# Kernel optimization log

Hardware: AMD Instinct MI355X
Metric: run time of the kernel (lower is better)

## Reference

```python
import jax, jax.numpy as jnp
import numpy as np

EPS = 1e-3  # keras BatchNormalization default epsilon


def _ngf(atoms, bonds, edges, W, b):
    """NeuralGraphHidden: neighbor gather + per-degree dense.
    atoms [B,N,Fa], bonds [B,N,D,Fb], edges [B,N,D] (-1 padded),
    W [D+1, Fa+Fb, width], b [D+1, width] -> [B,N,width]."""
    B, N, Fa = atoms.shape
    D = edges.shape[-1]
    deg = jnp.sum(edges != -1, axis=-1)  # [B,N] atom degrees
    # zero-row padded lookup table so edge index -1 gathers zeros
    apad = jnp.concatenate([jnp.zeros((B, 1, Fa), atoms.dtype), atoms], axis=1)
    neigh = jax.vmap(lambda a, e: a[e])(apad, edges + 1)  # [B,N,D,Fa]
    summed_atom = atoms + neigh.sum(axis=2)  # include_self=True
    summed_bond = bonds.sum(axis=2)
    feats = jnp.concatenate([summed_atom, summed_bond], axis=-1)  # [B,N,Fa+Fb]
    # dense transform for every degree, then select by actual degree
    all_out = jnp.einsum('bnf,dfw->bdnw', feats, W) + b[None, :, None, :]
    mask = (deg[:, None, :] == jnp.arange(D + 1)[None, :, None]).astype(atoms.dtype)
    return jnp.einsum('bdnw,bdn->bnw', all_out, mask)


def _bn(x, g, beta, m, v):
    return g * (x - m) * jax.lax.rsqrt(v + EPS) + beta


def setup_inputs() -> dict:
    key = jax.random.key(0)
    ks = jax.random.split(key, 32)
    B, N, D, Fa, Fb = 1024, 60, 5, 62, 6
    widths = [128, 128, 128]
    KSZ, FILT = 16, 128

    atoms = jax.random.normal(ks[0], (B, N, Fa), jnp.float32)
    bonds = jax.random.uniform(ks[1], (B, N, D, Fb), dtype=jnp.float32)
    edges = jax.random.randint(ks[2], (B, N, D), -1, N).astype(jnp.int32)

    def glorot(k, shape):
        s = jnp.sqrt(2.0 / (shape[-2] + shape[-1])).astype(jnp.float32)
        return jax.random.normal(k, shape, jnp.float32) * s

    inp = dict(atoms=atoms, bonds=bonds, edges=edges)
    fins = [Fa + Fb, widths[0] + Fb, widths[1] + Fb]
    for i in range(3):
        inp['W%d' % (i + 1)] = glorot(ks[3 + i], (D + 1, fins[i], widths[i]))
        inp['b%d' % (i + 1)] = 0.01 * jax.random.normal(ks[6 + i], (D + 1, widths[i]), jnp.float32)
    inp['Wc'] = glorot(ks[9], (KSZ, widths[2], FILT))
    for i, c in enumerate([widths[0], widths[1], widths[2], FILT]):
        inp['bn%d_g' % (i + 1)] = 1.0 + 0.1 * jax.random.normal(ks[10 + i], (c,), jnp.float32)
        inp['bn%d_b' % (i + 1)] = 0.1 * jax.random.normal(ks[14 + i], (c,), jnp.float32)
        inp['bn%d_m' % (i + 1)] = 0.1 * jax.random.normal(ks[18 + i], (c,), jnp.float32)
        inp['bn%d_v' % (i + 1)] = jax.random.uniform(ks[22 + i], (c,), jnp.float32, 0.5, 1.5)
    return inp


def reference(atoms, bonds, edges, W1, b1, W2, b2, W3, b3, Wc,
              bn1_g, bn1_b, bn1_m, bn1_v, bn2_g, bn2_b, bn2_m, bn2_v,
              bn3_g, bn3_b, bn3_m, bn3_v, bn4_g, bn4_b, bn4_m, bn4_v):
    x = jax.nn.relu(_bn(_ngf(atoms, bonds, edges, W1, b1), bn1_g, bn1_b, bn1_m, bn1_v))
    x = jax.nn.relu(_bn(_ngf(x, bonds, edges, W2, b2), bn2_g, bn2_b, bn2_m, bn2_v))
    x = jax.nn.relu(_bn(_ngf(x, bonds, edges, W3, b3), bn3_g, bn3_b, bn3_m, bn3_v))
    # Conv1D over the atom axis, VALID padding, no bias
    x = jax.lax.conv_general_dilated(x, Wc, window_strides=(1,), padding='VALID',
                                     dimension_numbers=('NWC', 'WIO', 'NWC'))
    x = jax.nn.relu(_bn(x, bn4_g, bn4_b, bn4_m, bn4_v))
    # dropout is identity at inference
    return x
```

## Files before the change

kernel.cpp:

```cpp
#include <hip/hip_runtime.h>
#include <hip/hip_bf16.h>

typedef __attribute__((ext_vector_type(8))) short bf16x8;
typedef __attribute__((ext_vector_type(4))) short short4v;
typedef __attribute__((ext_vector_type(4))) float f32x4;
typedef unsigned short u16;

static constexpr size_t OFF_BN   = 0;
static constexpr size_t OFF_SH2  = 4096;
static constexpr size_t OFF_BSUM = 13312;
static constexpr size_t OFF_WT1  = 750592;
static constexpr size_t OFF_WT2  = 898048;
static constexpr size_t OFF_WT3  = 1143808;
static constexpr size_t OFF_WCF  = 1389568;

__device__ __forceinline__ float bf2f(u16 r) {
  union { unsigned u; float f; } cv; cv.u = ((unsigned)r) << 16; return cv.f;
}
__device__ __forceinline__ u16 f2bf(float x) {
  __hip_bfloat16 h = __float2bfloat16(x); return *(u16*)&h;
}
__device__ __forceinline__ int xswz(int n, int c) {
  return n * 128 + ((((c >> 3) ^ (n & 7)) << 3) | (c & 7));
}
__device__ __forceinline__ int fswz(int n, int c) {
  return n * 160 + ((((c >> 3) ^ ((n >> 1) & 3)) << 3) | (c & 7));
}

__global__ __launch_bounds__(512) void bn_prep(
    const float* g1, const float* be1, const float* m1, const float* v1,
    const float* g2, const float* be2, const float* m2, const float* v2,
    const float* g3, const float* be3, const float* m3, const float* v3,
    const float* g4, const float* be4, const float* m4, const float* v4,
    const float* bb1, const float* bb2, const float* bb3,
    float* __restrict__ scale, float* __restrict__ shift,
    float* __restrict__ shift2) {
  int bid = blockIdx.x, t = threadIdx.x;
  if (bid == 0) {
    const float* gs[4] = {g1, g2, g3, g4};
    const float* bs[4] = {be1, be2, be3, be4};
    const float* ms[4] = {m1, m2, m3, m4};
    const float* vs[4] = {v1, v2, v3, v4};
    int l = t >> 7, ch = t & 127;
    float g = gs[l][ch], be = bs[l][ch], m = ms[l][ch], v = vs[l][ch];
    float sc = g / sqrtf(v + 1e-3f);
    scale[t] = sc;
    shift[t] = be - m * sc;
  } else if (t < 384) {
    int d = bid - 1;
    const float* gs[3] = {g1, g2, g3};
    const float* bs[3] = {be1, be2, be3};
    const float* ms[3] = {m1, m2, m3};
    const float* vs[3] = {v1, v2, v3};
    const float* bl[3] = {bb1, bb2, bb3};
    int ll = t >> 7, f = t & 127;
    float g = gs[ll][f], be = bs[ll][f], m = ms[ll][f], v = vs[ll][f];
    float sc = g / sqrtf(v + 1e-3f);
    float sh = be - m * sc;
    shift2[ll * 768 + d * 128 + f] = bl[ll][d * 128 + f] * sc + sh;
  }
}

__global__ __launch_bounds__(256) void bsum_prep(const float* __restrict__ bonds,
                                                 u16* __restrict__ bsum) {
  int a = blockIdx.x * 256 + threadIdx.x;
  const float* p = bonds + (size_t)a * 30;
  float s[6] = {0.f, 0.f, 0.f, 0.f, 0.f, 0.f};
  #pragma unroll
  for (int d = 0; d < 5; ++d)
    #pragma unroll
    for (int j = 0; j < 6; ++j) s[j] += p[d * 6 + j];
  #pragma unroll
  for (int j = 0; j < 6; ++j) bsum[(size_t)a * 6 + j] = f2bf(s[j]);
}

template <int FIN, int KSTEPS>
__global__ __launch_bounds__(256) void wtf_prep(const float* __restrict__ W,
                                                u16* __restrict__ wtf) {
  int v = blockIdx.x * 256 + threadIdx.x;
  if (v >= 6 * KSTEPS * 8 * 64) return;
  int lane = v & 63;
  int ftile = (v >> 6) & 7;
  int ks = (v >> 9) % KSTEPS;
  int d = (v >> 9) / KSTEPS;
  int f = ftile * 16 + (lane & 15);
  int k0 = ks * 32 + (lane >> 4) * 8;
  bf16x8 o;
  #pragma unroll
  for (int i = 0; i < 8; ++i) {
    int k = k0 + i;
    float x = (k < FIN) ? W[((size_t)d * FIN + k) * 128 + f] : 0.f;
    o[i] = (short)f2bf(x);
  }
  *reinterpret_cast<bf16x8*>(&wtf[(size_t)v * 8]) = o;
}

__global__ __launch_bounds__(512) void wcf_prep(const float* __restrict__ Wc,
                                                u16* __restrict__ wcf) {
  int v = blockIdx.x * 512 + threadIdx.x;
  int lane = v & 63;
  int ftile = (v >> 6) & 7;
  int ks = v >> 9;
  int f = ftile * 16 + (lane & 15);
  int k0 = ks * 32 + (lane >> 4) * 8;
  int tap = k0 >> 7, ch0 = k0 & 127;
  bf16x8 o;
  #pragma unroll
  for (int i = 0; i < 8; ++i)
    o[i] = (short)f2bf(Wc[((size_t)tap * 128 + ch0 + i) * 128 + f]);
  *reinterpret_cast<bf16x8*>(&wcf[(size_t)v * 8]) = o;
}

template <int CIN, int KSTEPS>
__device__ __forceinline__ void ngf_layer_dev(
    u16* __restrict__ xb, u16* __restrict__ feats,
    const int* __restrict__ eds, const int* __restrict__ degs,
    const int* __restrict__ presentS,
    const u16* __restrict__ bsum_b,
    const u16* __restrict__ wtf,
    const float* __restrict__ sc_l, const float* __restrict__ sh2_l,
    int tid, int lane, int wid) {
  constexpr int CW = (CIN <= 64) ? 64 : 128;
  for (int i = tid; i < 60 * CW; i += 256) {
    int n = i / CW, c = i % CW;
    if (c < CIN) {
      float v = bf2f(xb[xswz(n, c)]);
      #pragma unroll
      for (int d = 0; d < 5; ++d) {
        int e = eds[n * 5 + d];
        if (e >= 0) v += bf2f(xb[xswz(e, c)]);
      }
      feats[fswz(n, c)] = f2bf(v);
    }
  }
  for (int i = tid; i < 360; i += 256) {
    int n = i / 6, c = CIN + (i % 6);
    feats[fswz(n, c)] = bsum_b[i];
  }
  __syncthreads();

  const int pres = *presentS;
  const int rgrp = lane >> 4;
  const int fr = lane & 15;
  const int f0 = wid * 32;

  for (int d = 0; d < 6; ++d) {
    if (!(pres & (1 << d))) continue;
    f32x4 acc[4][2];
    #pragma unroll
    for (int mt = 0; mt < 4; ++mt)
      #pragma unroll
      for (int nt = 0; nt < 2; ++nt) acc[mt][nt] = (f32x4){0.f, 0.f, 0.f, 0.f};
    const u16* __restrict__ wd = wtf + (size_t)d * KSTEPS * 4096;
    bf16x8 bcur[2], bnxt[2];
    #pragma unroll
    for (int nt = 0; nt < 2; ++nt)
      bcur[nt] = *reinterpret_cast<const bf16x8*>(
          &wd[(((size_t)0 * 8 + wid * 2 + nt) * 64 + lane) * 8]);
    #pragma unroll
    for (int ks = 0; ks < KSTEPS; ++ks) {
      if (ks + 1 < KSTEPS) {
        #pragma unroll
        for (int nt = 0; nt < 2; ++nt)
          bnxt[nt] = *reinterpret_cast<const bf16x8*>(
              &wd[((((size_t)ks + 1) * 8 + wid * 2 + nt) * 64 + lane) * 8]);
      }
      bf16x8 a[4];
      #pragma unroll
      for (int mt = 0; mt < 4; ++mt) {
        int r = mt * 16 + fr;
        int u = (ks * 4 + rgrp) ^ ((fr >> 1) & 3);
        a[mt] = *reinterpret_cast<const bf16x8*>(&feats[r * 160 + u * 8]);
      }
      #pragma unroll
      for (int mt = 0; mt < 4; ++mt)
        #pragma unroll
        for (int nt = 0; nt < 2; ++nt)
          acc[mt][nt] = __builtin_amdgcn_mfma_f32_16x16x32_bf16(a[mt], bcur[nt],
                                                                acc[mt][nt], 0, 0, 0);
      #pragma unroll
      for (int nt = 0; nt < 2; ++nt) bcur[nt] = bnxt[nt];
    }
    float s0 = sc_l[f0 + fr],      h0 = sh2_l[d * 128 + f0 + fr];
    float s1 = sc_l[f0 + 16 + fr], h1 = sh2_l[d * 128 + f0 + 16 + fr];
    #pragma unroll
    for (int mt = 0; mt < 4; ++mt) {
      #pragma unroll
      for (int j = 0; j < 4; ++j) {
        int n = mt * 16 + rgrp * 4 + j;
        if (n < 60 && degs[n] == d) {
          xb[xswz(n, f0 + fr)]      = f2bf(fmaxf(acc[mt][0][j] * s0 + h0, 0.f));
          xb[xswz(n, f0 + 16 + fr)] = f2bf(fmaxf(acc[mt][1][j] * s1 + h1, 0.f));
        }
      }
    }
  }
  __syncthreads();
}

__global__ __launch_bounds__(256, 4) void mega(
    const float* __restrict__ atoms, const int* __restrict__ edges_g,
    const u16* __restrict__ bsum, const u16* __restrict__ wt1,
    const u16* __restrict__ wt2, const u16* __restrict__ wt3,
    const u16* __restrict__ wcf, const float* __restrict__ scale,
    const float* __restrict__ shift, const float* __restrict__ shift2,
    float* __restrict__ out) {
  __shared__ u16 xb[64 * 128];
  __shared__ u16 feats[64 * 160];
  __shared__ int eds[300];
  __shared__ int degs[64];
  __shared__ int presentS;
  const int b = blockIdx.x, tid = threadIdx.x;
  const int lane = tid & 63;
  const int wid = __builtin_amdgcn_readfirstlane(tid >> 6);

  if (tid == 0) presentS = 0;
  for (int i = tid; i < 300; i += 256) eds[i] = edges_g[b * 300 + i];
  {
    short4v* fz = (short4v*)feats;
    for (int i = tid; i < 64 * 160 / 4; i += 256) fz[i] = (short4v){0, 0, 0, 0};
  }
  for (int i = tid; i < 60 * 64; i += 256) {
    int n = i >> 6, c = i & 63;
    if (c < 62) xb[xswz(n, c)] = f2bf(atoms[(size_t)b * 3720 + n * 62 + c]);
  }
  __syncthreads();

  if (tid < 64) {
    int dg = 7;
    if (tid < 60) {
      dg = 0;
      #pragma unroll
      for (int d = 0; d < 5; ++d) dg += (eds[tid * 5 + d] >= 0);
      atomicOr(&presentS, 1 << dg);
    }
    degs[tid] = dg;
  }

  const u16* bsum_b = bsum + (size_t)b * 360;
  ngf_layer_dev<62, 3>(xb, feats, eds, degs, &presentS, bsum_b, wt1,
                       scale + 0, shift2 + 0, tid, lane, wid);
  ngf_layer_dev<128, 5>(xb, feats, eds, degs, &presentS, bsum_b, wt2,
                        scale + 128, shift2 + 768, tid, lane, wid);
  ngf_layer_dev<128, 5>(xb, feats, eds, degs, &presentS, bsum_b, wt3,
                        scale + 256, shift2 + 1536, tid, lane, wid);

  {
    const int fr = lane & 15;
    const int rgrp = lane >> 4;
    const int f0 = wid * 32;
    f32x4 cacc[3][2];
    #pragma unroll
    for (int rt = 0; rt < 3; ++rt)
      #pragma unroll
      for (int ct = 0; ct < 2; ++ct) cacc[rt][ct] = (f32x4){0.f, 0.f, 0.f, 0.f};

    bf16x8 br[2][2], ar[2][3];
    auto loadB = [&](int ks, int slot) {
      #pragma unroll
      for (int nt = 0; nt < 2; ++nt)
        br[slot][nt] = *reinterpret_cast<const bf16x8*>(
            &wcf[(((size_t)ks * 8 + wid * 2 + nt) * 64 + lane) * 8]);
    };
    auto loadA = [&](int ks, int slot) {
      int rowadd = ks >> 2;
      int unit = ((ks & 3) << 2) + rgrp;
      #pragma unroll
      for (int rt = 0; rt < 3; ++rt) {
        int arow = rt * 16 + fr + rowadd;
        int uo = unit ^ (arow & 7);
        ar[slot][rt] = *reinterpret_cast<const bf16x8*>(&xb[arow * 128 + uo * 8]);
      }
    };
    loadB(0, 0); loadB(1, 1); loadA(0, 0);
    #pragma unroll 2
    for (int ks = 0; ks < 64; ++ks) {
      if (ks < 63) loadA(ks + 1, (ks + 1) & 1);
      #pragma unroll
      for (int rt = 0; rt < 3; ++rt)
        #pragma unroll
        for (int ct = 0; ct < 2; ++ct)
          cacc[rt][ct] = __builtin_amdgcn_mfma_f32_16x16x32_bf16(
              ar[ks & 1][rt], br[ks & 1][ct], cacc[rt][ct], 0, 0, 0);
      if (ks < 62) loadB(ks + 2, ks & 1);
    }

    #pragma unroll
    for (int ct = 0; ct < 2; ++ct) {
      int f = f0 + ct * 16 + fr;
      float sc = scale[384 + f], sh = shift[384 + f];
      #pragma unroll
      for (int rt = 0; rt < 3; ++rt) {
        #pragma unroll
        for (int j = 0; j < 4; ++j) {
          int t = rt * 16 + rgrp * 4 + j;
          if (t < 45) {
            float y = fmaxf(cacc[rt][ct][j] * sc + sh, 0.f);
            out[((size_t)b * 45 + t) * 128 + f] = y;
          }
        }
      }
    }
  }
}

extern "C" void kernel_launch(void* const* d_in, const int* in_sizes, int n_in,
                              void* d_out, int out_size, void* d_ws, size_t ws_size,
                              hipStream_t stream) {
  const float* atoms = (const float*)d_in[0];
  const float* bonds = (const float*)d_in[1];
  const int*   edges = (const int*)d_in[2];
  const float* W1 = (const float*)d_in[3]; const float* b1 = (const float*)d_in[4];
  const float* W2 = (const float*)d_in[5]; const float* b2 = (const float*)d_in[6];
  const float* W3 = (const float*)d_in[7]; const float* b3 = (const float*)d_in[8];
  const float* Wc = (const float*)d_in[9];

  char* ws = (char*)d_ws;
  float* scale  = (float*)(ws + OFF_BN);
  float* shift  = scale + 512;
  float* shift2 = (float*)(ws + OFF_SH2);
  u16*   bsum   = (u16*)(ws + OFF_BSUM);
  u16*   wt1    = (u16*)(ws + OFF_WT1);
  u16*   wt2    = (u16*)(ws + OFF_WT2);
  u16*   wt3    = (u16*)(ws + OFF_WT3);
  u16*   wcf    = (u16*)(ws + OFF_WCF);

  bn_prep<<<7, 512, 0, stream>>>(
      (const float*)d_in[10], (const float*)d_in[11], (const float*)d_in[12], (const float*)d_in[13],
      (const float*)d_in[14], (const float*)d_in[15], (const float*)d_in[16], (const float*)d_in[17],
      (const float*)d_in[18], (const float*)d_in[19], (const float*)d_in[20], (const float*)d_in[21],
      (const float*)d_in[22], (const float*)d_in[23], (const float*)d_in[24], (const float*)d_in[25],
      b1, b2, b3, scale, shift, shift2);
  bsum_prep<<<240, 256, 0, stream>>>(bonds, bsum);
  wcf_prep<<<64, 512, 0, stream>>>(Wc, wcf);
  wtf_prep<68, 3><<<36, 256, 0, stream>>>(W1, wt1);
  wtf_prep<134, 5><<<60, 256, 0, stream>>>(W2, wt2);
  wtf_prep<134, 5><<<60, 256, 0, stream>>>(W3, wt3);

  mega<<<1024, 256, 0, stream>>>(atoms, edges, bsum, wt1, wt2, wt3, wcf,
                                 scale, shift, shift2, (float*)d_out);
}
```

Measured before the change: 218.6 us.

## Replace scalar neighbor gather with adjacency-matrix MFMA and fuse prep kernels

The per-element neighbor gather-sum is replaced by building a per-molecule 60x60 adjacency count matrix (self plus edges) in shared memory and computing the aggregation as a bf16 MFMA matmul against a transposed activation buffer. The per-degree dense stage is transposed (weights as the A operand, features as B), the layer-3 output is written in the row layout the conv expects, and edges and degrees are stored as bytes to shrink shared memory. The six preprocessing launches are merged into one kernel, and the bond sums are staged through shared memory. Rounding the aggregated sums to bf16 before the dense stage slightly changes numerics.

```diff
diff --git a/kernel.cpp b/kernel.cpp
--- a/kernel.cpp
+++ b/kernel.cpp
@@ -5,6 +5,7 @@
 typedef __attribute__((ext_vector_type(4))) short short4v;
 typedef __attribute__((ext_vector_type(4))) float f32x4;
 typedef unsigned short u16;
+typedef unsigned char u8;
 
 static constexpr size_t OFF_BN   = 0;
 static constexpr size_t OFF_SH2  = 4096;
@@ -20,65 +21,12 @@
 __device__ __forceinline__ u16 f2bf(float x) {
   __hip_bfloat16 h = __float2bfloat16(x); return *(u16*)&h;
 }
-__device__ __forceinline__ int xswz(int n, int c) {
-  return n * 128 + ((((c >> 3) ^ (n & 7)) << 3) | (c & 7));
-}
-__device__ __forceinline__ int fswz(int n, int c) {
-  return n * 160 + ((((c >> 3) ^ ((n >> 1) & 3)) << 3) | (c & 7));
-}
-
-__global__ __launch_bounds__(512) void bn_prep(
-    const float* g1, const float* be1, const float* m1, const float* v1,
-    const float* g2, const float* be2, const float* m2, const float* v2,
-    const float* g3, const float* be3, const float* m3, const float* v3,
-    const float* g4, const float* be4, const float* m4, const float* v4,
-    const float* bb1, const float* bb2, const float* bb3,
-    float* __restrict__ scale, float* __restrict__ shift,
-    float* __restrict__ shift2) {
-  int bid = blockIdx.x, t = threadIdx.x;
-  if (bid == 0) {
-    const float* gs[4] = {g1, g2, g3, g4};
-    const float* bs[4] = {be1, be2, be3, be4};
-    const float* ms[4] = {m1, m2, m3, m4};
-    const float* vs[4] = {v1, v2, v3, v4};
-    int l = t >> 7, ch = t & 127;
-    float g = gs[l][ch], be = bs[l][ch], m = ms[l][ch], v = vs[l][ch];
-    float sc = g / sqrtf(v + 1e-3f);
-    scale[t] = sc;
-    shift[t] = be - m * sc;
-  } else if (t < 384) {
-    int d = bid - 1;
-    const float* gs[3] = {g1, g2, g3};
-    const float* bs[3] = {be1, be2, be3};
-    const float* ms[3] = {m1, m2, m3};
-    const float* vs[3] = {v1, v2, v3};
-    const float* bl[3] = {bb1, bb2, bb3};
-    int ll = t >> 7, f = t & 127;
-    float g = gs[ll][f], be = bs[ll][f], m = ms[ll][f], v = vs[ll][f];
-    float sc = g / sqrtf(v + 1e-3f);
-    float sh = be - m * sc;
-    shift2[ll * 768 + d * 128 + f] = bl[ll][d * 128 + f] * sc + sh;
-  }
-}
-
-__global__ __launch_bounds__(256) void bsum_prep(const float* __restrict__ bonds,
-                                                 u16* __restrict__ bsum) {
-  int a = blockIdx.x * 256 + threadIdx.x;
-  const float* p = bonds + (size_t)a * 30;
-  float s[6] = {0.f, 0.f, 0.f, 0.f, 0.f, 0.f};
-  #pragma unroll
-  for (int d = 0; d < 5; ++d)
-    #pragma unroll
-    for (int j = 0; j < 6; ++j) s[j] += p[d * 6 + j];
-  #pragma unroll
-  for (int j = 0; j < 6; ++j) bsum[(size_t)a * 6 + j] = f2bf(s[j]);
-}
-
-template <int FIN, int KSTEPS>
-__global__ __launch_bounds__(256) void wtf_prep(const float* __restrict__ W,
-                                                u16* __restrict__ wtf) {
-  int v = blockIdx.x * 256 + threadIdx.x;
-  if (v >= 6 * KSTEPS * 8 * 64) return;
+__device__ __forceinline__ int xts(int c, int n) {
+  return c * 64 + (((n >> 3) ^ (c & 7)) << 3) + (n & 7);
+}
+
+__device__ __forceinline__ void emit_wt(u16* dst, const float* W, int FIN, int FIN_A,
+                                        int CB, int KSTEPS, int v) {
   int lane = v & 63;
   int ftile = (v >> 6) & 7;
   int ks = (v >> 9) % KSTEPS;
@@ -89,108 +37,222 @@
   #pragma unroll
   for (int i = 0; i < 8; ++i) {
     int k = k0 + i;
-    float x = (k < FIN) ? W[((size_t)d * FIN + k) * 128 + f] : 0.f;
+    int src = (k < FIN_A) ? k : (k >= CB && k < CB + 6) ? (FIN_A + k - CB) : -1;
+    float x = (src >= 0) ? W[((size_t)d * FIN + src) * 128 + f] : 0.f;
     o[i] = (short)f2bf(x);
   }
-  *reinterpret_cast<bf16x8*>(&wtf[(size_t)v * 8]) = o;
-}
-
-__global__ __launch_bounds__(512) void wcf_prep(const float* __restrict__ Wc,
-                                                u16* __restrict__ wcf) {
-  int v = blockIdx.x * 512 + threadIdx.x;
-  int lane = v & 63;
-  int ftile = (v >> 6) & 7;
-  int ks = v >> 9;
-  int f = ftile * 16 + (lane & 15);
-  int k0 = ks * 32 + (lane >> 4) * 8;
-  int tap = k0 >> 7, ch0 = k0 & 127;
-  bf16x8 o;
-  #pragma unroll
-  for (int i = 0; i < 8; ++i)
-    o[i] = (short)f2bf(Wc[((size_t)tap * 128 + ch0 + i) * 128 + f]);
-  *reinterpret_cast<bf16x8*>(&wcf[(size_t)v * 8]) = o;
-}
-
-template <int CIN, int KSTEPS>
-__device__ __forceinline__ void ngf_layer_dev(
-    u16* __restrict__ xb, u16* __restrict__ feats,
-    const int* __restrict__ eds, const int* __restrict__ degs,
-    const int* __restrict__ presentS,
-    const u16* __restrict__ bsum_b,
-    const u16* __restrict__ wtf,
-    const float* __restrict__ sc_l, const float* __restrict__ sh2_l,
-    int tid, int lane, int wid) {
-  constexpr int CW = (CIN <= 64) ? 64 : 128;
-  for (int i = tid; i < 60 * CW; i += 256) {
-    int n = i / CW, c = i % CW;
-    if (c < CIN) {
-      float v = bf2f(xb[xswz(n, c)]);
-      #pragma unroll
-      for (int d = 0; d < 5; ++d) {
-        int e = eds[n * 5 + d];
-        if (e >= 0) v += bf2f(xb[xswz(e, c)]);
-      }
-      feats[fswz(n, c)] = f2bf(v);
+  *reinterpret_cast<bf16x8*>(&dst[(size_t)v * 8]) = o;
+}
+
+__global__ __launch_bounds__(256) void prep(
+    const float* __restrict__ bonds, const float* __restrict__ Wc,
+    const float* __restrict__ W1, const float* __restrict__ W2, const float* __restrict__ W3,
+    const float* g1, const float* be1, const float* m1, const float* v1,
+    const float* g2, const float* be2, const float* m2, const float* v2,
+    const float* g3, const float* be3, const float* m3, const float* v3,
+    const float* g4, const float* be4, const float* m4, const float* v4,
+    const float* bb1, const float* bb2, const float* bb3,
+    float* __restrict__ scale, float* __restrict__ shift, float* __restrict__ shift2,
+    u16* __restrict__ bsum, u16* __restrict__ wt1, u16* __restrict__ wt2,
+    u16* __restrict__ wt3, u16* __restrict__ wcf) {
+  __shared__ float sb[3840];
+  const int b = blockIdx.x, tid = threadIdx.x;
+  if (b < 480) {
+    const int base = b * 128;
+    const float4* src = (const float4*)(bonds + (size_t)base * 30);
+    for (int i = tid; i < 960; i += 256) ((float4*)sb)[i] = src[i];
+    __syncthreads();
+    if (tid < 128) {
+      float s[6] = {0.f, 0.f, 0.f, 0.f, 0.f, 0.f};
+      #pragma unroll
+      for (int d = 0; d < 5; ++d)
+        #pragma unroll
+        for (int j = 0; j < 6; ++j) s[j] += sb[tid * 30 + d * 6 + j];
+      #pragma unroll
+      for (int j = 0; j < 6; ++j) bsum[(size_t)(base + tid) * 6 + j] = f2bf(s[j]);
+    }
+  } else if (b < 608) {
+    int v = (b - 480) * 256 + tid;
+    int lane = v & 63, ftile = (v >> 6) & 7, ks = v >> 9;
+    int f = ftile * 16 + (lane & 15);
+    int k0 = ks * 32 + (lane >> 4) * 8;
+    int tap = k0 >> 7, ch0 = k0 & 127;
+    bf16x8 o;
+    #pragma unroll
+    for (int i = 0; i < 8; ++i)
+      o[i] = (short)f2bf(Wc[((size_t)tap * 128 + ch0 + i) * 128 + f]);
+    *reinterpret_cast<bf16x8*>(&wcf[(size_t)v * 8]) = o;
+  } else if (b < 644) {
+    emit_wt(wt1, W1, 68, 62, 64, 3, (b - 608) * 256 + tid);
+  } else if (b < 704) {
+    emit_wt(wt2, W2, 134, 128, 128, 5, (b - 644) * 256 + tid);
+  } else if (b < 764) {
+    emit_wt(wt3, W3, 134, 128, 128, 5, (b - 704) * 256 + tid);
+  } else if (b < 766) {
+    int idx = (b - 764) * 256 + tid;
+    const float* gs[4] = {g1, g2, g3, g4};
+    const float* bs[4] = {be1, be2, be3, be4};
+    const float* ms[4] = {m1, m2, m3, m4};
+    const float* vs[4] = {v1, v2, v3, v4};
+    int l = idx >> 7, ch = idx & 127;
+    float sc = gs[l][ch] / sqrtf(vs[l][ch] + 1e-3f);
+    scale[idx] = sc;
+    shift[idx] = bs[l][ch] - ms[l][ch] * sc;
+  } else {
+    int i = (b - 766) * 256 + tid;
+    if (i < 2304) {
+      const float* G[3] = {g1, g2, g3};
+      const float* Be[3] = {be1, be2, be3};
+      const float* M[3] = {m1, m2, m3};
+      const float* V[3] = {v1, v2, v3};
+      const float* Bl[3] = {bb1, bb2, bb3};
+      int ll = i / 768, r = i % 768, f = r & 127;
+      float sc = G[ll][f] / sqrtf(V[ll][f] + 1e-3f);
+      float sh = Be[ll][f] - M[ll][f] * sc;
+      shift2[i] = Bl[ll][r] * sc + sh;
+    }
+  }
+}
+
+template <int MPW, int CB, int KSTEPS, bool TOCONV>
+__device__ __forceinline__ void layer(
+    u16* __restrict__ feats, u16* __restrict__ xbt,
+    const u8* __restrict__ S8, const u8* __restrict__ degs8,
+    const int* __restrict__ presentS, const u16* __restrict__ bsum_b,
+    const u16* __restrict__ wtf, const float* __restrict__ sc_l,
+    const float* __restrict__ sh2_l, int tid, int lane, int wid) {
+  const int fr = lane & 15, rg = lane >> 4;
+
+  bf16x8 sf[4][2];
+  #pragma unroll
+  for (int nt = 0; nt < 4; ++nt) {
+    #pragma unroll
+    for (int ks = 0; ks < 2; ++ks) {
+      int n = nt * 16 + fr, m0 = ks * 32 + rg * 8;
+      const unsigned* wp = (const unsigned*)(S8 + n * 64 + m0);
+      unsigned lo = wp[0], hi = wp[1];
+      bf16x8 v;
+      #pragma unroll
+      for (int i = 0; i < 4; ++i) v[i] = (short)f2bf((float)((lo >> (i * 8)) & 255u));
+      #pragma unroll
+      for (int i = 0; i < 4; ++i) v[4 + i] = (short)f2bf((float)((hi >> (i * 8)) & 255u));
+      sf[nt][ks] = v;
+    }
+  }
+
+  f32x4 gacc[MPW][4];
+  #pragma unroll
+  for (int mt = 0; mt < MPW; ++mt)
+    #pragma unroll
+    for (int nt = 0; nt < 4; ++nt) gacc[mt][nt] = (f32x4){0.f, 0.f, 0.f, 0.f};
+  #pragma unroll
+  for (int mt = 0; mt < MPW; ++mt) {
+    const int c = (wid * MPW + mt) * 16 + fr;
+    #pragma unroll
+    for (int ks = 0; ks < 2; ++ks) {
+      const int m0 = ks * 32 + rg * 8;
+      bf16x8 a = *reinterpret_cast<const bf16x8*>(
+          &xbt[c * 64 + (((m0 >> 3) ^ (c & 7)) << 3)]);
+      #pragma unroll
+      for (int nt = 0; nt < 4; ++nt)
+        gacc[mt][nt] = __builtin_amdgcn_mfma_f32_16x16x32_bf16(a, sf[nt][ks],
+                                                               gacc[mt][nt], 0, 0, 0);
+    }
+  }
+  #pragma unroll
+  for (int mt = 0; mt < MPW; ++mt) {
+    const int c0 = (wid * MPW + mt) * 16 + rg * 4;
+    const int uu = c0 >> 3;
+    #pragma unroll
+    for (int nt = 0; nt < 4; ++nt) {
+      const int n = nt * 16 + fr;
+      if (n < 60) {
+        short4v p;
+        #pragma unroll
+        for (int j = 0; j < 4; ++j) p[j] = (short)f2bf(gacc[mt][nt][j]);
+        *reinterpret_cast<short4v*>(
+            &feats[n * 160 + ((uu ^ (n & 7)) << 3) + (c0 & 7)]) = p;
+      }
     }
   }
   for (int i = tid; i < 360; i += 256) {
-    int n = i / 6, c = CIN + (i % 6);
-    feats[fswz(n, c)] = bsum_b[i];
+    int n = i / 6, c = CB + (i % 6);
+    int u = c >> 3;
+    int uu2 = (u < 16) ? (u ^ (n & 7)) : u;
+    feats[n * 160 + (uu2 << 3) + (c & 7)] = bsum_b[i];
   }
   __syncthreads();
 
   const int pres = *presentS;
-  const int rgrp = lane >> 4;
-  const int fr = lane & 15;
-  const int f0 = wid * 32;
+  int dg[4];
+  #pragma unroll
+  for (int nt = 0; nt < 4; ++nt) dg[nt] = degs8[nt * 16 + fr];
+  float4 scv[2];
+  #pragma unroll
+  for (int mt = 0; mt < 2; ++mt)
+    scv[mt] = *reinterpret_cast<const float4*>(&sc_l[(wid * 2 + mt) * 16 + rg * 4]);
 
   for (int d = 0; d < 6; ++d) {
     if (!(pres & (1 << d))) continue;
-    f32x4 acc[4][2];
-    #pragma unroll
-    for (int mt = 0; mt < 4; ++mt)
-      #pragma unroll
-      for (int nt = 0; nt < 2; ++nt) acc[mt][nt] = (f32x4){0.f, 0.f, 0.f, 0.f};
+    f32x4 acc[2][4];
+    #pragma unroll
+    for (int mt = 0; mt < 2; ++mt)
+      #pragma unroll
+      for (int nt = 0; nt < 4; ++nt) acc[mt][nt] = (f32x4){0.f, 0.f, 0.f, 0.f};
     const u16* __restrict__ wd = wtf + (size_t)d * KSTEPS * 4096;
-    bf16x8 bcur[2], bnxt[2];
-    #pragma unroll
-    for (int nt = 0; nt < 2; ++nt)
-      bcur[nt] = *reinterpret_cast<const bf16x8*>(
-          &wd[(((size_t)0 * 8 + wid * 2 + nt) * 64 + lane) * 8]);
+    bf16x8 acur[2], anxt[2];
+    #pragma unroll
+    for (int mt = 0; mt < 2; ++mt)
+      acur[mt] = *reinterpret_cast<const bf16x8*>(
+          &wd[((0 * 8 + wid * 2 + mt) * 64 + lane) * 8]);
     #pragma unroll
     for (int ks = 0; ks < KSTEPS; ++ks) {
       if (ks + 1 < KSTEPS) {
         #pragma unroll
-        for (int nt = 0; nt < 2; ++nt)
-          bnxt[nt] = *reinterpret_cast<const bf16x8*>(
-              &wd[((((size_t)ks + 1) * 8 + wid * 2 + nt) * 64 + lane) * 8]);
-      }
-      bf16x8 a[4];
-      #pragma unroll
-      for (int mt = 0; mt < 4; ++mt) {
-        int r = mt * 16 + fr;
-        int u = (ks * 4 + rgrp) ^ ((fr >> 1) & 3);
-        a[mt] = *reinterpret_cast<const bf16x8*>(&feats[r * 160 + u * 8]);
-      }
-      #pragma unroll
-      for (int mt = 0; mt < 4; ++mt)
-        #pragma unroll
-        for (int nt = 0; nt < 2; ++nt)
-          acc[mt][nt] = __builtin_amdgcn_mfma_f32_16x16x32_bf16(a[mt], bcur[nt],
+        for (int mt = 0; mt < 2; ++mt)
+          anxt[mt] = *reinterpret_cast<const bf16x8*>(
+              &wd[(((ks + 1) * 8 + wid * 2 + mt) * 64 + lane) * 8]);
+      }
+      bf16x8 bfr[4];
+      const int u = (ks * 32 + rg * 8) >> 3;
+      #pragma unroll
+      for (int nt = 0; nt < 4; ++nt) {
+        const int n = nt * 16 + fr;
+        const int uu2 = (u < 16) ? (u ^ (n & 7)) : u;
+        bfr[nt] = *reinterpret_cast<const bf16x8*>(&feats[n * 160 + (uu2 << 3)]);
+      }
+      #pragma unroll
+      for (int mt = 0; mt < 2; ++mt)
+        #pragma unroll
+        for (int nt = 0; nt < 4; ++nt)
+          acc[mt][nt] = __builtin_amdgcn_mfma_f32_16x16x32_bf16(acur[mt], bfr[nt],
                                                                 acc[mt][nt], 0, 0, 0);
       #pragma unroll
-      for (int nt = 0; nt < 2; ++nt) bcur[nt] = bnxt[nt];
-    }
-    float s0 = sc_l[f0 + fr],      h0 = sh2_l[d * 128 + f0 + fr];
-    float s1 = sc_l[f0 + 16 + fr], h1 = sh2_l[d * 128 + f0 + 16 + fr];
-    #pragma unroll
-    for (int mt = 0; mt < 4; ++mt) {
-      #pragma unroll
-      for (int j = 0; j < 4; ++j) {
-        int n = mt * 16 + rgrp * 4 + j;
-        if (n < 60 && degs[n] == d) {
-          xb[xswz(n, f0 + fr)]      = f2bf(fmaxf(acc[mt][0][j] * s0 + h0, 0.f));
-          xb[xswz(n, f0 + 16 + fr)] = f2bf(fmaxf(acc[mt][1][j] * s1 + h1, 0.f));
+      for (int mt = 0; mt < 2; ++mt) acur[mt] = anxt[mt];
+    }
+    #pragma unroll
+    for (int mt = 0; mt < 2; ++mt) {
+      const int f0 = (wid * 2 + mt) * 16 + rg * 4;
+      float4 shv = *reinterpret_cast<const float4*>(&sh2_l[d * 128 + f0]);
+      #pragma unroll
+      for (int nt = 0; nt < 4; ++nt) {
+        const int n = nt * 16 + fr;
+        if (n < 60 && dg[nt] == d) {
+          float y0 = fmaxf(acc[mt][nt][0] * scv[mt].x + shv.x, 0.f);
+          float y1 = fmaxf(acc[mt][nt][1] * scv[mt].y + shv.y, 0.f);
+          float y2 = fmaxf(acc[mt][nt][2] * scv[mt].z + shv.z, 0.f);
+          float y3 = fmaxf(acc[mt][nt][3] * scv[mt].w + shv.w, 0.f);
+          if (TOCONV) {
+            short4v p = {(short)f2bf(y0), (short)f2bf(y1),
+                         (short)f2bf(y2), (short)f2bf(y3)};
+            *reinterpret_cast<short4v*>(
+                &xbt[n * 128 + (((f0 >> 3) ^ (n & 7)) << 3) + (f0 & 7)]) = p;
+          } else {
+            xbt[xts(f0 + 0, n)] = f2bf(y0);
+            xbt[xts(f0 + 1, n)] = f2bf(y1);
+            xbt[xts(f0 + 2, n)] = f2bf(y2);
+            xbt[xts(f0 + 3, n)] = f2bf(y3);
+          }
         }
       }
     }
@@ -205,50 +267,58 @@
     const u16* __restrict__ wcf, const float* __restrict__ scale,
     const float* __restrict__ shift, const float* __restrict__ shift2,
     float* __restrict__ out) {
-  __shared__ u16 xb[64 * 128];
-  __shared__ u16 feats[64 * 160];
-  __shared__ int eds[300];
-  __shared__ int degs[64];
-  __shared__ int presentS;
+  __shared__ __align__(16) char smem[39808];
+  u16* feats = (u16*)smem;
+  u16* xbt = (u16*)(smem + 19200);
+  u8* S8 = (u8*)(smem + 35584);
+  signed char* eds = (signed char*)(smem + 39424);
+  u8* degs8 = (u8*)(smem + 39728);
+  int* presentS = (int*)(smem + 39792);
+
   const int b = blockIdx.x, tid = threadIdx.x;
   const int lane = tid & 63;
   const int wid = __builtin_amdgcn_readfirstlane(tid >> 6);
 
-  if (tid == 0) presentS = 0;
-  for (int i = tid; i < 300; i += 256) eds[i] = edges_g[b * 300 + i];
+  if (tid == 0) *presentS = 0;
+  for (int i = tid; i < 1200; i += 256) ((int4*)feats)[i] = (int4){0, 0, 0, 0};
+  for (int i = tid; i < 240; i += 256) ((int4*)S8)[i] = (int4){0, 0, 0, 0};
+  for (int i = tid; i < 300; i += 256) eds[i] = (signed char)edges_g[b * 300 + i];
+  for (int i = tid; i < 8192; i += 256) {
+    int n = i >> 7, c = i & 127;
+    float x = (c < 62 && n < 60) ? atoms[(size_t)b * 3720 + n * 62 + c] : 0.f;
+    xbt[xts(c, n)] = f2bf(x);
+  }
+  __syncthreads();
+
+  if (tid < 64) {
+    int dgv = 7;
+    if (tid < 60) {
+      dgv = 0;
+      #pragma unroll
+      for (int d = 0; d < 5; ++d) dgv += (eds[tid * 5 + d] >= 0);
+      atomicOr(presentS, 1 << dgv);
+      S8[tid * 64 + tid] = (u8)(S8[tid * 64 + tid] + 1);
+      #pragma unroll
+      for (int d = 0; d < 5; ++d) {
+        int e = eds[tid * 5 + d];
+        if (e >= 0) S8[tid * 64 + e] = (u8)(S8[tid * 64 + e] + 1);
+      }
+    }
+    degs8[tid] = (u8)dgv;
+  }
+  __syncthreads();
+
+  const u16* bsum_b = bsum + (size_t)b * 360;
+  layer<1, 64, 3, false>(feats, xbt, S8, degs8, presentS, bsum_b, wt1,
+                         scale + 0, shift2 + 0, tid, lane, wid);
+  layer<2, 128, 5, false>(feats, xbt, S8, degs8, presentS, bsum_b, wt2,
+                          scale + 128, shift2 + 768, tid, lane, wid);
+  layer<2, 128, 5, true>(feats, xbt, S8, degs8, presentS, bsum_b, wt3,
+                         scale + 256, shift2 + 1536, tid, lane, wid);
+
   {
-    short4v* fz = (short4v*)feats;
-    for (int i = tid; i < 64 * 160 / 4; i += 256) fz[i] = (short4v){0, 0, 0, 0};
-  }
-  for (int i = tid; i < 60 * 64; i += 256) {
-    int n = i >> 6, c = i & 63;
-    if (c < 62) xb[xswz(n, c)] = f2bf(atoms[(size_t)b * 3720 + n * 62 + c]);
-  }
-  __syncthreads();
-
-  if (tid < 64) {
-    int dg = 7;
-    if (tid < 60) {
-      dg = 0;
-      #pragma unroll
-      for (int d = 0; d < 5; ++d) dg += (eds[tid * 5 + d] >= 0);
-      atomicOr(&presentS, 1 << dg);
-    }
-    degs[tid] = dg;
-  }
-
-  const u16* bsum_b = bsum + (size_t)b * 360;
-  ngf_layer_dev<62, 3>(xb, feats, eds, degs, &presentS, bsum_b, wt1,
-                       scale + 0, shift2 + 0, tid, lane, wid);
-  ngf_layer_dev<128, 5>(xb, feats, eds, degs, &presentS, bsum_b, wt2,
-                        scale + 128, shift2 + 768, tid, lane, wid);
-  ngf_layer_dev<128, 5>(xb, feats, eds, degs, &presentS, bsum_b, wt3,
-                        scale + 256, shift2 + 1536, tid, lane, wid);
-
-  {
-    const int fr = lane & 15;
-    const int rgrp = lane >> 4;
-    const int f0 = wid * 32;
+    const int fr = lane & 15, rg = lane >> 4;
+    const u16* xconv = xbt;
     f32x4 cacc[3][2];
     #pragma unroll
     for (int rt = 0; rt < 3; ++rt)
@@ -264,12 +334,12 @@
     };
     auto loadA = [&](int ks, int slot) {
       int rowadd = ks >> 2;
-      int unit = ((ks & 3) << 2) + rgrp;
+      int unit = ((ks & 3) << 2) + rg;
       #pragma unroll
       for (int rt = 0; rt < 3; ++rt) {
         int arow = rt * 16 + fr + rowadd;
         int uo = unit ^ (arow & 7);
-        ar[slot][rt] = *reinterpret_cast<const bf16x8*>(&xb[arow * 128 + uo * 8]);
+        ar[slot][rt] = *reinterpret_cast<const bf16x8*>(&xconv[arow * 128 + uo * 8]);
       }
     };
     loadB(0, 0); loadB(1, 1); loadA(0, 0);
@@ -287,13 +357,13 @@
 
     #pragma unroll
     for (int ct = 0; ct < 2; ++ct) {
-      int f = f0 + ct * 16 + fr;
+      int f = wid * 32 + ct * 16 + fr;
       float sc = scale[384 + f], sh = shift[384 + f];
       #pragma unroll
       for (int rt = 0; rt < 3; ++rt) {
         #pragma unroll
         for (int j = 0; j < 4; ++j) {
-          int t = rt * 16 + rgrp * 4 + j;
+          int t = rt * 16 + rg * 4 + j;
           if (t < 45) {
             float y = fmaxf(cacc[rt][ct][j] * sc + sh, 0.f);
             out[((size_t)b * 45 + t) * 128 + f] = y;
@@ -325,17 +395,13 @@
   u16*   wt3    = (u16*)(ws + OFF_WT3);
   u16*   wcf    = (u16*)(ws + OFF_WCF);
 
-  bn_prep<<<7, 512, 0, stream>>>(
+  prep<<<775, 256, 0, stream>>>(
+      bonds, Wc, W1, W2, W3,
       (const float*)d_in[10], (const float*)d_in[11], (const float*)d_in[12], (const float*)d_in[13],
       (const float*)d_in[14], (const float*)d_in[15], (const float*)d_in[16], (const float*)d_in[17],
       (const float*)d_in[18], (const float*)d_in[19], (const float*)d_in[20], (const float*)d_in[21],
       (const float*)d_in[22], (const float*)d_in[23], (const float*)d_in[24], (const float*)d_in[25],
-      b1, b2, b3, scale, shift, shift2);
-  bsum_prep<<<240, 256, 0, stream>>>(bonds, bsum);
-  wcf_prep<<<64, 512, 0, stream>>>(Wc, wcf);
-  wtf_prep<68, 3><<<36, 256, 0, stream>>>(W1, wt1);
-  wtf_prep<134, 5><<<60, 256, 0, stream>>>(W2, wt2);
-  wtf_prep<134, 5><<<60, 256, 0, stream>>>(W3, wt3);
+      b1, b2, b3, scale, shift, shift2, bsum, wt1, wt2, wt3, wcf);
 
   mega<<<1024, 256, 0, stream>>>(atoms, edges, bsum, wt1, wt2, wt3, wcf,
                                  scale, shift, shift2, (float*)d_out);
```

After: 215.9 us. Within noise of the previous version (-1.2%).
